# Kernel optimization log

Hardware: AMD Instinct MI355X
Metric: run time of the kernel (lower is better)

## Reference

```python
import jax, jax.numpy as jnp
import numpy as np

NUM_HEADS = 16
NUM_FEATURES = 1024
HEAD_DIM = NUM_FEATURES // NUM_HEADS
B, S = 2, 2048


def setup_inputs() -> dict:
    key = jax.random.key(0)
    ks = jax.random.split(key, 12)
    d = NUM_FEATURES
    scale = 1.0 / np.sqrt(d)
    inp = {
        'q': jax.random.normal(ks[0], (B, S, d), jnp.float32),
        'v': jax.random.normal(ks[1], (B, S, d), jnp.float32),
        'k': jax.random.normal(ks[2], (B, S, d), jnp.float32),
        'mask': jnp.ones((1, 1, S, S), jnp.float32),
        # Dense params: flax kernel layout (in, out)
        'Wq': jax.random.normal(ks[3], (d, d), jnp.float32) * scale,
        'bq': jnp.zeros((d,), jnp.float32),
        'Wv': jax.random.normal(ks[4], (d, d), jnp.float32) * scale,
        'bv': jnp.zeros((d,), jnp.float32),
        'Wk': jax.random.normal(ks[5], (d, d), jnp.float32) * scale,
        'bk': jnp.zeros((d,), jnp.float32),
        'Wo': jax.random.normal(ks[6], (d, d), jnp.float32) * scale,
        'bo': jnp.zeros((d,), jnp.float32),
    }
    return inp


def _split_heads(x):
    b, s, _ = x.shape
    return jnp.transpose(x.reshape(b, s, NUM_HEADS, HEAD_DIM), (0, 2, 1, 3))  # [B,H,S,Dh]


def reference(q, v, k, mask, Wq, bq, Wv, bv, Wk, bk, Wo, bo):
    q = q @ Wq + bq
    v = v @ Wv + bv
    k = k @ Wk + bk
    qh = _split_heads(q) / jnp.sqrt(jnp.float32(NUM_FEATURES))  # note: sqrt(d_model), as in source
    kh = _split_heads(k)
    vh = _split_heads(v)
    logits = jnp.einsum('bhqd,bhkd->bhqk', qh, kh)
    logits = logits - 1e9 * (1.0 - mask)
    weights = jax.nn.softmax(logits, axis=-1)
    # dropout deterministic (eval_mode=True) -> identity
    out = jnp.einsum('bhqk,bhkd->bhqd', weights, vh)
    out = jnp.transpose(out, (0, 2, 1, 3)).reshape(q.shape[0], q.shape[1], NUM_FEATURES)
    return out @ Wo + bo
```

## Files before the change

### kernel.cpp

```cpp
#include <hip/hip_runtime.h>
#include <hip/hip_bf16.h>


namespace {
constexpr int DM = 1024;
constexpr int NH = 16;
constexpr int HD = 64;
constexpr int SQ = 2048;
constexpr int M_TOT = 2 * SQ;

using f32x4  = __attribute__((ext_vector_type(4))) float;
using f32x16 = __attribute__((ext_vector_type(16))) float;
using bf16x8 = __attribute__((ext_vector_type(8))) short;
using u16 = unsigned short;

__device__ __forceinline__ u16 f2bf(float f) {
  union { float f; unsigned u; } x; x.f = f;
  unsigned r = x.u + 0x7fffu + ((x.u >> 16) & 1u);
  return (u16)(r >> 16);
}

__device__ __forceinline__ unsigned pk2(float lo, float hi) {
  unsigned r;
  asm("v_cvt_pk_bf16_f32 %0, %1, %2" : "=v"(r) : "v"(lo), "v"(hi));
  return r;
}

__device__ __forceinline__ float fexp2(float x) {
  float r;
  asm("v_exp_f32 %0, %1" : "=v"(r) : "v"(x));
  return r;
}

__device__ __forceinline__ f32x16 mfma32(bf16x8 a, bf16x8 b, f32x16 c) {
  return __builtin_amdgcn_mfma_f32_32x32x16_bf16(a, b, c, 0, 0, 0);
}

__device__ __forceinline__ void gld16(const void* g, void* l) {
  __builtin_amdgcn_global_load_lds((const __attribute__((address_space(1))) void*)g,
                                   (__attribute__((address_space(3))) void*)l, 16, 0, 0);
}
}

__global__ __launch_bounds__(256) void tobf_kernel(const float* __restrict__ q,
                                                   const float* __restrict__ k,
                                                   const float* __restrict__ v,
                                                   u16* __restrict__ out) {
  const float* src = blockIdx.y == 0 ? q : (blockIdx.y == 1 ? k : v);
  u16* dst = out + (size_t)blockIdx.y * M_TOT * DM;
  size_t i = ((size_t)blockIdx.x * 256 + threadIdx.x) * 8;
  float4 a = *(const float4*)(src + i), b = *(const float4*)(src + i + 4);
  union { u16 us[8]; uint4 v4; } pk;
  pk.us[0] = f2bf(a.x); pk.us[1] = f2bf(a.y); pk.us[2] = f2bf(a.z); pk.us[3] = f2bf(a.w);
  pk.us[4] = f2bf(b.x); pk.us[5] = f2bf(b.y); pk.us[6] = f2bf(b.z); pk.us[7] = f2bf(b.w);
  *(uint4*)(dst + i) = pk.v4;
}

__global__ __launch_bounds__(256) void wtrans4_kernel(const float* __restrict__ Wq,
                                                      const float* __restrict__ Wk,
                                                      const float* __restrict__ Wv,
                                                      const float* __restrict__ Wo,
                                                      u16* __restrict__ W3t,
                                                      u16* __restrict__ Wot) {
  const int z = blockIdx.z;
  const float* W = z == 0 ? Wq : (z == 1 ? Wk : (z == 2 ? Wv : Wo));
  u16* Wt = z < 3 ? W3t + (size_t)z * DM * DM : Wot;
  __shared__ u16 tile[64][65];
  const int t = threadIdx.x;
  const int k0 = blockIdx.y * 64, n0 = blockIdx.x * 64;
#pragma unroll
  for (int i = 0; i < 16; ++i) {
    int flat = t + i * 256;
    int kk = flat >> 6, nn = flat & 63;
    tile[kk][nn] = f2bf(W[(size_t)(k0 + kk) * DM + n0 + nn]);
  }
  __syncthreads();
#pragma unroll
  for (int i = 0; i < 16; ++i) {
    int flat = t + i * 256;
    int nn = flat >> 6, kk = flat & 63;
    Wt[(size_t)(n0 + nn) * DM + k0 + kk] = tile[kk][nn];
  }
}

__global__ __launch_bounds__(256) void vtrans_kernel(const u16* __restrict__ Vh,
                                                     u16* __restrict__ Vt) {
  __shared__ u16 tile[64][80];
  const int s0 = blockIdx.x * 64, bh = blockIdx.y;
  const u16* src = Vh + ((size_t)bh * SQ + s0) * HD;
  u16* dst = Vt + (size_t)bh * HD * SQ + s0;
  const int t = threadIdx.x;
#pragma unroll
  for (int i = 0; i < 2; ++i) {
    int flat = t + i * 256;
    int sr = flat >> 3, ch = flat & 7;
    *(uint4*)&tile[sr][ch * 8] = *(const uint4*)&src[(size_t)sr * HD + ch * 8];
  }
  __syncthreads();
#pragma unroll
  for (int i = 0; i < 2; ++i) {
    int flat = t + i * 256;
    int dh = flat >> 3, ch = flat & 7;
    union { u16 us[8]; uint2 h[2]; } pk;
#pragma unroll
    for (int j = 0; j < 8; ++j) pk.us[j] = tile[ch * 8 + j][dh];
#pragma unroll
    for (int kq = 0; kq < 2; ++kq) {
      int g = ch * 2 + kq;
      int gl = (g & ~3) | ((g & 1) << 1) | ((g & 2) >> 1);
      *(uint2*)&dst[(size_t)dh * SQ + gl * 4] = pk.h[kq];
    }
  }
}

template <int EPI>
__device__ __forceinline__ void gemm_core(const u16* __restrict__ A,
                                          const u16* __restrict__ Wt,
                                          const float* __restrict__ bias,
                                          void* __restrict__ C, float scale,
                                          int m0, int n0, u16* ldsA, u16* ldsB) {
  const int t = threadIdx.x;
  const int lane = t & 63, w = t >> 6;
  const int wm = w >> 1, wn = w & 1;
  const int c = lane & 15, g = lane >> 4;
  const int lr = lane >> 3, lc = lane & 7;
  f32x4 acc[2][4] = {};

  for (int k0 = 0; k0 < DM; k0 += 64) {
    __syncthreads();
#pragma unroll
    for (int j = 0; j < 2; ++j) {
      int row = w * 16 + j * 8 + lr;
      int gc = lc ^ (row & 7);
      gld16(&A[(size_t)(m0 + row) * DM + k0 + gc * 8], (char*)ldsA + w * 2048 + j * 1024);
    }
#pragma unroll
    for (int j = 0; j < 4; ++j) {
      int row = w * 32 + j * 8 + lr;
      int gc = lc ^ (row & 7);
      gld16(&Wt[(size_t)(n0 + row) * DM + k0 + gc * 8], (char*)ldsB + w * 4096 + j * 1024);
    }
    __syncthreads();
#pragma unroll
    for (int ks = 0; ks < 2; ++ks) {
      bf16x8 af[2], bfr[4];
#pragma unroll
      for (int mi = 0; mi < 2; ++mi) {
        int R = wm * 32 + mi * 16 + c;
        af[mi] = *(const bf16x8*)((const char*)ldsA + R * 128 + ((4 * ks + g) ^ (R & 7)) * 16);
      }
#pragma unroll
      for (int ni = 0; ni < 4; ++ni) {
        int R = wn * 64 + ni * 16 + c;
        bfr[ni] = *(const bf16x8*)((const char*)ldsB + R * 128 + ((4 * ks + g) ^ (R & 7)) * 16);
      }
#pragma unroll
      for (int mi = 0; mi < 2; ++mi)
#pragma unroll
        for (int ni = 0; ni < 4; ++ni)
          acc[mi][ni] =
              __builtin_amdgcn_mfma_f32_16x16x32_bf16(af[mi], bfr[ni], acc[mi][ni], 0, 0, 0);
    }
  }
  float bv_[4];
#pragma unroll
  for (int ni = 0; ni < 4; ++ni) bv_[ni] = bias[n0 + wn * 64 + ni * 16 + c];
#pragma unroll
  for (int mi = 0; mi < 2; ++mi)
#pragma unroll
    for (int ni = 0; ni < 4; ++ni)
#pragma unroll
      for (int r = 0; r < 4; ++r) {
        int m = m0 + wm * 32 + mi * 16 + g * 4 + r;
        int n = n0 + wn * 64 + ni * 16 + c;
        float val = acc[mi][ni][r] + bv_[ni];
        if (EPI == 2) {
          ((float*)C)[(size_t)m * DM + n] = val;
        } else {
          int b = m >> 11, s = m & (SQ - 1);
          int h = n >> 6, dh = n & (HD - 1);
          ((u16*)C)[((size_t)(b * NH + h) * SQ + s) * HD + dh] = f2bf(val * scale);
        }
      }
}

__global__ __launch_bounds__(256) void qkvgemm_kernel(const u16* __restrict__ QKVbf,
                                                      const u16* __restrict__ W3t,
                                                      const float* __restrict__ bq,
                                                      const float* __restrict__ bk,
                                                      const float* __restrict__ bv,
                                                      u16* __restrict__ Qh,
                                                      u16* __restrict__ Kh,
                                                      u16* __restrict__ Vh) {
  __shared__ __align__(16) u16 ldsA[64 * 64];
  __shared__ __align__(16) u16 ldsB[128 * 64];
  int bid = blockIdx.x;
  int swz = (bid & 7) * 192 + (bid >> 3);
  int which = swz >> 9;
  int sub = swz & 511;
  int mt = sub >> 3, nt = sub & 7;
  const u16* A = QKVbf + (size_t)which * M_TOT * DM;
  const u16* Wt = W3t + (size_t)which * DM * DM;
  const float* bias = which == 0 ? bq : (which == 1 ? bk : bv);
  u16* C = which == 0 ? Qh : (which == 1 ? Kh : Vh);
  float scale = which == 0 ? 0.045084222f : 1.0f;
  gemm_core<0>(A, Wt, bias, C, scale, mt * 64, nt * 128, ldsA, ldsB);
}

__global__ __launch_bounds__(256) void ogemm_kernel(const u16* __restrict__ Ob,
                                                    const u16* __restrict__ Wot,
                                                    const float* __restrict__ bo,
                                                    float* __restrict__ out) {
  __shared__ __align__(16) u16 ldsA[64 * 64];
  __shared__ __align__(16) u16 ldsB[128 * 64];
  int bid = blockIdx.x;
  int swz = (bid & 7) * 64 + (bid >> 3);
  int mt = swz >> 3, nt = swz & 7;
  gemm_core<2>(Ob, Wot, bo, out, 1.0f, mt * 64, nt * 128, ldsA, ldsB);
}

__global__ __launch_bounds__(512, 4) void fattn_kernel(const u16* __restrict__ Qh,
                                                       const u16* __restrict__ Kh,
                                                       const u16* __restrict__ Vt,
                                                       u16* __restrict__ Ob) {
  __shared__ __align__(16) u16 ldsKV[2][2][2][64 * 64];
  __shared__ float ldsML[2][8][32];
  const int t = threadIdx.x;
  const int lane = t & 63, w = t >> 6;
  const int l31 = lane & 31, hi = lane >> 5;
  const int wq = w >> 1, wk = w & 1;

  const int bid = blockIdx.x;
  const int swz = (bid & 7) * 64 + (bid >> 3);
  const int bh = swz >> 4, qb = swz & 15;
  const int q0 = qb * 128 + wq * 32;
  const u16* Qb = Qh + (size_t)bh * SQ * HD;
  const u16* Kb = Kh + (size_t)bh * SQ * HD;
  const u16* Vb = Vt + (size_t)bh * HD * SQ;
  const int keybase = wk * (SQ / 2);

  bf16x8 qf[4];
#pragma unroll
  for (int ks = 0; ks < 4; ++ks)
    qf[ks] = *(const bf16x8*)&Qb[(size_t)(q0 + l31) * HD + ks * 16 + hi * 8];

  f32x16 o0 = {}, o1 = {};
  float m_run = -3e38f, l_run = 0.f;

  auto stage = [&](int kt, int buf) {
#pragma unroll
    for (int j = 0; j < 2; ++j) {
      int r = j * 32 + wq * 8 + (lane >> 3);
      int cg = (lane & 7) ^ (r & 7);
      gld16(&Kb[(size_t)(keybase + kt * 64 + r) * HD + cg * 8],
            (char*)&ldsKV[wk][buf][0][0] + j * 4096 + wq * 1024);
      gld16(&Vb[(size_t)r * SQ + keybase + kt * 64 + cg * 8],
            (char*)&ldsKV[wk][buf][1][0] + j * 4096 + wq * 1024);
    }
  };

  stage(0, 0);
  __syncthreads();

  for (int kt = 0; kt < 16; ++kt) {
    const int cur = kt & 1;
    if (kt + 1 < 16) stage(kt + 1, cur ^ 1);

    f32x16 s0 = {}, s1 = {};
    const char* kbp = (const char*)&ldsKV[wk][cur][0][0];
#pragma unroll
    for (int ks = 0; ks < 4; ++ks) {
      int ch = ((ks * 2 + hi) ^ (l31 & 7)) * 16;
      bf16x8 k0 = *(const bf16x8*)(kbp + l31 * 128 + ch);
      bf16x8 k1 = *(const bf16x8*)(kbp + (32 + l31) * 128 + ch);
      s0 = mfma32(k0, qf[ks], s0);
      s1 = mfma32(k1, qf[ks], s1);
    }

    float mx[16];
#pragma unroll
    for (int r = 0; r < 16; ++r) mx[r] = fmaxf(s0[r], s1[r]);
#pragma unroll
    for (int d = 8; d >= 1; d >>= 1)
#pragma unroll
      for (int r = 0; r < d; ++r) mx[r] = fmaxf(mx[r], mx[r + d]);
    float pmax = fmaxf(mx[0], __shfl_xor(mx[0], 32));

    if (__any(pmax > m_run + 8.0f)) {
      float mnew = fmaxf(m_run, pmax);
      float scf = fexp2(m_run - mnew);
      m_run = mnew;
      l_run *= scf;
#pragma unroll
      for (int r = 0; r < 16; ++r) {
        float sv = __shfl(scf, (r & 3) + 8 * (r >> 2) + 4 * hi);
        o0[r] *= sv;
        o1[r] *= sv;
      }
    }
#pragma unroll
    for (int r = 0; r < 16; ++r) {
      s0[r] = fexp2(s0[r] - m_run);
      s1[r] = fexp2(s1[r] - m_run);
    }
    float sm[16];
#pragma unroll
    for (int r = 0; r < 16; ++r) sm[r] = s0[r] + s1[r];
#pragma unroll
    for (int d = 8; d >= 1; d >>= 1)
#pragma unroll
      for (int r = 0; r < d; ++r) sm[r] += sm[r + d];
    l_run += sm[0];

    union W8 { unsigned u[4]; bf16x8 v; };
    W8 pa[4];
#pragma unroll
    for (int wd = 0; wd < 4; ++wd) {
      pa[0].u[wd] = pk2(s0[2 * wd], s0[2 * wd + 1]);
      pa[1].u[wd] = pk2(s0[8 + 2 * wd], s0[9 + 2 * wd]);
      pa[2].u[wd] = pk2(s1[2 * wd], s1[2 * wd + 1]);
      pa[3].u[wd] = pk2(s1[8 + 2 * wd], s1[9 + 2 * wd]);
    }

    const char* vbp = (const char*)&ldsKV[wk][cur][1][0];
#pragma unroll
    for (int g = 0; g < 4; ++g) {
      int ch = ((g * 2 + hi) ^ (l31 & 7)) * 16;
      bf16x8 v0 = *(const bf16x8*)(vbp + l31 * 128 + ch);
      bf16x8 v1 = *(const bf16x8*)(vbp + (32 + l31) * 128 + ch);
      o0 = mfma32(pa[g].v, v0, o0);
      o1 = mfma32(pa[g].v, v1, o1);
    }

    __syncthreads();
  }

  float l2 = l_run + __shfl_xor(l_run, 32);
  float (*ldsO)[32][64] = (float(*)[32][64]) & ldsKV[0][0][0][0];
#pragma unroll
  for (int r = 0; r < 16; ++r) {
    int q = (r & 3) + 8 * (r >> 2) + 4 * hi;
    ldsO[w][q][l31] = o0[r];
    ldsO[w][q][32 + l31] = o1[r];
  }
  if (hi == 0) {
    ldsML[0][w][l31] = m_run;
    ldsML[1][w][l31] = l2;
  }
  __syncthreads();

  {
    const int q = t >> 2;
    const int dh0 = (t & 3) * 16;
    const int wA = (q >> 5) * 2;
    const int ql = q & 31;
    float m0 = ldsML[0][wA][ql], m1 = ldsML[0][wA + 1][ql];
    float l0 = ldsML[1][wA][ql], l1 = ldsML[1][wA + 1][ql];
    float mxv = fmaxf(m0, m1);
    float f0 = fexp2(m0 - mxv), f1 = fexp2(m1 - mxv);
    float inv = 1.0f / (l0 * f0 + l1 * f1);
    union { u16 us[16]; uint4 v4[2]; } pk;
#pragma unroll
    for (int j = 0; j < 16; ++j)
      pk.us[j] = f2bf((ldsO[wA][ql][dh0 + j] * f0 + ldsO[wA + 1][ql][dh0 + j] * f1) * inv);
    const int b = bh >> 4, h = bh & (NH - 1);
    size_t base = ((size_t)b * SQ + qb * 128 + q) * DM + h * HD + dh0;
    *(uint4*)&Ob[base] = pk.v4[0];
    *(uint4*)&Ob[base + 8] = pk.v4[1];
  }
}

extern "C" void kernel_launch(void* const* d_in, const int* in_sizes, int n_in,
                              void* d_out, int out_size, void* d_ws, size_t ws_size,
                              hipStream_t stream) {
  (void)in_sizes; (void)n_in; (void)out_size; (void)ws_size;
  const float* q  = (const float*)d_in[0];
  const float* v  = (const float*)d_in[1];
  const float* k  = (const float*)d_in[2];
  const float* Wq = (const float*)d_in[4];
  const float* bq = (const float*)d_in[5];
  const float* Wv = (const float*)d_in[6];
  const float* bv = (const float*)d_in[7];
  const float* Wk = (const float*)d_in[8];
  const float* bk = (const float*)d_in[9];
  const float* Wo = (const float*)d_in[10];
  const float* bo = (const float*)d_in[11];

  char* ws = (char*)d_ws;
  const size_t MB = 1024 * 1024;
  u16* W3t   = (u16*)(ws + 0 * MB);
  u16* Wot   = (u16*)(ws + 6 * MB);
  u16* QKVbf = (u16*)(ws + 8 * MB);
  u16* Vh    = (u16*)(ws + 32 * MB);
  u16* Vt    = (u16*)(ws + 8 * MB);
  u16* Ob    = (u16*)(ws + 16 * MB);
  u16* Qh    = (u16*)d_out;
  u16* Kh    = (u16*)d_out + (size_t)4 * 1024 * 1024;

  const dim3 blk(256);
  tobf_kernel<<<dim3(2048, 3), blk, 0, stream>>>(q, k, v, QKVbf);

  wtrans4_kernel<<<dim3(16, 16, 4), blk, 0, stream>>>(Wq, Wk, Wv, Wo, W3t, Wot);

  qkvgemm_kernel<<<dim3(1536), blk, 0, stream>>>(QKVbf, W3t, bq, bk, bv, Qh, Kh, Vh);

  vtrans_kernel<<<dim3(32, 32), blk, 0, stream>>>(Vh, Vt);

  fattn_kernel<<<dim3(512), dim3(512), 0, stream>>>(Qh, Kh, Vt, Ob);

  ogemm_kernel<<<dim3(512), blk, 0, stream>>>(Ob, Wot, bo, (float*)d_out);
}
```

Measured before the change: 125.8 us.

## Fuse V transpose into QKV GEMM epilogue and compute softmax row sums via MFMA

The V projection GEMM now writes its output directly in the transposed, permuted Vt layout, which removes the separate vtrans kernel launch and one round trip of V through memory. In the attention kernel, the row max reduction uses v_max3 instructions. The row-sum accumulation is moved onto the matrix cores by multiplying P with a ones vector, replacing the VALU add-reduction. The transposed epilogue stores are strided 8-byte writes, and the extra MFMAs add matrix-core work to each tile iteration.

```diff
diff --git a/kernel.cpp b/kernel.cpp
--- a/kernel.cpp
+++ b/kernel.cpp
@@ -29,6 +29,12 @@
 __device__ __forceinline__ float fexp2(float x) {
   float r;
   asm("v_exp_f32 %0, %1" : "=v"(r) : "v"(x));
+  return r;
+}
+
+__device__ __forceinline__ float m3(float a, float b, float c) {
+  float r;
+  asm("v_max3_f32 %0, %1, %2, %3" : "=v"(r) : "v"(a), "v"(b), "v"(c));
   return r;
 }
 
@@ -83,36 +89,6 @@
   }
 }
 
-__global__ __launch_bounds__(256) void vtrans_kernel(const u16* __restrict__ Vh,
-                                                     u16* __restrict__ Vt) {
-  __shared__ u16 tile[64][80];
-  const int s0 = blockIdx.x * 64, bh = blockIdx.y;
-  const u16* src = Vh + ((size_t)bh * SQ + s0) * HD;
-  u16* dst = Vt + (size_t)bh * HD * SQ + s0;
-  const int t = threadIdx.x;
-#pragma unroll
-  for (int i = 0; i < 2; ++i) {
-    int flat = t + i * 256;
-    int sr = flat >> 3, ch = flat & 7;
-    *(uint4*)&tile[sr][ch * 8] = *(const uint4*)&src[(size_t)sr * HD + ch * 8];
-  }
-  __syncthreads();
-#pragma unroll
-  for (int i = 0; i < 2; ++i) {
-    int flat = t + i * 256;
-    int dh = flat >> 3, ch = flat & 7;
-    union { u16 us[8]; uint2 h[2]; } pk;
-#pragma unroll
-    for (int j = 0; j < 8; ++j) pk.us[j] = tile[ch * 8 + j][dh];
-#pragma unroll
-    for (int kq = 0; kq < 2; ++kq) {
-      int g = ch * 2 + kq;
-      int gl = (g & ~3) | ((g & 1) << 1) | ((g & 2) >> 1);
-      *(uint2*)&dst[(size_t)dh * SQ + gl * 4] = pk.h[kq];
-    }
-  }
-}
-
 template <int EPI>
 __device__ __forceinline__ void gemm_core(const u16* __restrict__ A,
                                           const u16* __restrict__ Wt,
@@ -166,22 +142,36 @@
 #pragma unroll
   for (int ni = 0; ni < 4; ++ni) bv_[ni] = bias[n0 + wn * 64 + ni * 16 + c];
 #pragma unroll
-  for (int mi = 0; mi < 2; ++mi)
-#pragma unroll
-    for (int ni = 0; ni < 4; ++ni)
-#pragma unroll
-      for (int r = 0; r < 4; ++r) {
-        int m = m0 + wm * 32 + mi * 16 + g * 4 + r;
+  for (int mi = 0; mi < 2; ++mi) {
+#pragma unroll
+    for (int ni = 0; ni < 4; ++ni) {
+      if (EPI == 1) {
+        int mbase = m0 + wm * 32 + mi * 16 + g * 4;
         int n = n0 + wn * 64 + ni * 16 + c;
-        float val = acc[mi][ni][r] + bv_[ni];
-        if (EPI == 2) {
-          ((float*)C)[(size_t)m * DM + n] = val;
-        } else {
-          int b = m >> 11, s = m & (SQ - 1);
-          int h = n >> 6, dh = n & (HD - 1);
-          ((u16*)C)[((size_t)(b * NH + h) * SQ + s) * HD + dh] = f2bf(val * scale);
+        int b = mbase >> 11, s = mbase & (SQ - 1);
+        int sp = (s & ~12) | ((s & 4) << 1) | ((s & 8) >> 1);
+        int h = n >> 6, dh = n & (HD - 1);
+        uint2 pkd;
+        pkd.x = pk2(acc[mi][ni][0] + bv_[ni], acc[mi][ni][1] + bv_[ni]);
+        pkd.y = pk2(acc[mi][ni][2] + bv_[ni], acc[mi][ni][3] + bv_[ni]);
+        *(uint2*)&((u16*)C)[((size_t)(b * NH + h) * HD + dh) * SQ + sp] = pkd;
+      } else {
+#pragma unroll
+        for (int r = 0; r < 4; ++r) {
+          int m = m0 + wm * 32 + mi * 16 + g * 4 + r;
+          int n = n0 + wn * 64 + ni * 16 + c;
+          float val = acc[mi][ni][r] + bv_[ni];
+          if (EPI == 2) {
+            ((float*)C)[(size_t)m * DM + n] = val;
+          } else {
+            int b = m >> 11, s = m & (SQ - 1);
+            int h = n >> 6, dh = n & (HD - 1);
+            ((u16*)C)[((size_t)(b * NH + h) * SQ + s) * HD + dh] = f2bf(val * scale);
+          }
         }
       }
+    }
+  }
 }
 
 __global__ __launch_bounds__(256) void qkvgemm_kernel(const u16* __restrict__ QKVbf,
@@ -191,7 +181,7 @@
                                                       const float* __restrict__ bv,
                                                       u16* __restrict__ Qh,
                                                       u16* __restrict__ Kh,
-                                                      u16* __restrict__ Vh) {
+                                                      u16* __restrict__ Vt) {
   __shared__ __align__(16) u16 ldsA[64 * 64];
   __shared__ __align__(16) u16 ldsB[128 * 64];
   int bid = blockIdx.x;
@@ -201,10 +191,13 @@
   int mt = sub >> 3, nt = sub & 7;
   const u16* A = QKVbf + (size_t)which * M_TOT * DM;
   const u16* Wt = W3t + (size_t)which * DM * DM;
-  const float* bias = which == 0 ? bq : (which == 1 ? bk : bv);
-  u16* C = which == 0 ? Qh : (which == 1 ? Kh : Vh);
-  float scale = which == 0 ? 0.045084222f : 1.0f;
-  gemm_core<0>(A, Wt, bias, C, scale, mt * 64, nt * 128, ldsA, ldsB);
+  if (which == 0) {
+    gemm_core<0>(A, Wt, bq, Qh, 0.045084222f, mt * 64, nt * 128, ldsA, ldsB);
+  } else if (which == 1) {
+    gemm_core<0>(A, Wt, bk, Kh, 1.0f, mt * 64, nt * 128, ldsA, ldsB);
+  } else {
+    gemm_core<1>(A, Wt, bv, Vt, 1.0f, mt * 64, nt * 128, ldsA, ldsB);
+  }
 }
 
 __global__ __launch_bounds__(256) void ogemm_kernel(const u16* __restrict__ Ob,
@@ -244,8 +237,12 @@
   for (int ks = 0; ks < 4; ++ks)
     qf[ks] = *(const bf16x8*)&Qb[(size_t)(q0 + l31) * HD + ks * 16 + hi * 8];
 
+  const short ob = (short)0x3F80;
+  const bf16x8 onesv = {ob, ob, ob, ob, ob, ob, ob, ob};
+
   f32x16 o0 = {}, o1 = {};
-  float m_run = -3e38f, l_run = 0.f;
+  f32x16 lacc = {};
+  float m_run = -3e38f;
 
   auto stage = [&](int kt, int buf) {
 #pragma unroll
@@ -277,25 +274,27 @@
       s1 = mfma32(k1, qf[ks], s1);
     }
 
-    float mx[16];
-#pragma unroll
-    for (int r = 0; r < 16; ++r) mx[r] = fmaxf(s0[r], s1[r]);
-#pragma unroll
-    for (int d = 8; d >= 1; d >>= 1)
-#pragma unroll
-      for (int r = 0; r < d; ++r) mx[r] = fmaxf(mx[r], mx[r + d]);
-    float pmax = fmaxf(mx[0], __shfl_xor(mx[0], 32));
+    float t0 = m3(s0[0], s0[1], s0[2]),    t1 = m3(s0[3], s0[4], s0[5]);
+    float t2 = m3(s0[6], s0[7], s0[8]),    t3 = m3(s0[9], s0[10], s0[11]);
+    float t4 = m3(s0[12], s0[13], s0[14]), t5 = m3(s0[15], s1[0], s1[1]);
+    float t6 = m3(s1[2], s1[3], s1[4]),    t7 = m3(s1[5], s1[6], s1[7]);
+    float t8 = m3(s1[8], s1[9], s1[10]),   t9 = m3(s1[11], s1[12], s1[13]);
+    float t10 = fmaxf(s1[14], s1[15]);
+    float u0 = m3(t0, t1, t2), u1 = m3(t3, t4, t5), u2 = m3(t6, t7, t8);
+    float u3 = fmaxf(t9, t10);
+    float lm = fmaxf(m3(u0, u1, u2), u3);
+    float pmax = fmaxf(lm, __shfl_xor(lm, 32));
 
     if (__any(pmax > m_run + 8.0f)) {
       float mnew = fmaxf(m_run, pmax);
       float scf = fexp2(m_run - mnew);
       m_run = mnew;
-      l_run *= scf;
 #pragma unroll
       for (int r = 0; r < 16; ++r) {
         float sv = __shfl(scf, (r & 3) + 8 * (r >> 2) + 4 * hi);
         o0[r] *= sv;
         o1[r] *= sv;
+        lacc[r] *= sv;
       }
     }
 #pragma unroll
@@ -303,14 +302,6 @@
       s0[r] = fexp2(s0[r] - m_run);
       s1[r] = fexp2(s1[r] - m_run);
     }
-    float sm[16];
-#pragma unroll
-    for (int r = 0; r < 16; ++r) sm[r] = s0[r] + s1[r];
-#pragma unroll
-    for (int d = 8; d >= 1; d >>= 1)
-#pragma unroll
-      for (int r = 0; r < d; ++r) sm[r] += sm[r + d];
-    l_run += sm[0];
 
     union W8 { unsigned u[4]; bf16x8 v; };
     W8 pa[4];
@@ -321,6 +312,11 @@
       pa[2].u[wd] = pk2(s1[2 * wd], s1[2 * wd + 1]);
       pa[3].u[wd] = pk2(s1[8 + 2 * wd], s1[9 + 2 * wd]);
     }
+
+    lacc = mfma32(pa[0].v, onesv, lacc);
+    lacc = mfma32(pa[1].v, onesv, lacc);
+    lacc = mfma32(pa[2].v, onesv, lacc);
+    lacc = mfma32(pa[3].v, onesv, lacc);
 
     const char* vbp = (const char*)&ldsKV[wk][cur][1][0];
 #pragma unroll
@@ -335,7 +331,6 @@
     __syncthreads();
   }
 
-  float l2 = l_run + __shfl_xor(l_run, 32);
   float (*ldsO)[32][64] = (float(*)[32][64]) & ldsKV[0][0][0][0];
 #pragma unroll
   for (int r = 0; r < 16; ++r) {
@@ -343,9 +338,11 @@
     ldsO[w][q][l31] = o0[r];
     ldsO[w][q][32 + l31] = o1[r];
   }
-  if (hi == 0) {
-    ldsML[0][w][l31] = m_run;
-    ldsML[1][w][l31] = l2;
+  if (hi == 0) ldsML[0][w][l31] = m_run;
+  if (l31 == 0) {
+#pragma unroll
+    for (int r = 0; r < 16; ++r)
+      ldsML[1][w][(r & 3) + 8 * (r >> 2) + 4 * hi] = lacc[r];
   }
   __syncthreads();
 
@@ -391,8 +388,7 @@
   u16* W3t   = (u16*)(ws + 0 * MB);
   u16* Wot   = (u16*)(ws + 6 * MB);
   u16* QKVbf = (u16*)(ws + 8 * MB);
-  u16* Vh    = (u16*)(ws + 32 * MB);
-  u16* Vt    = (u16*)(ws + 8 * MB);
+  u16* Vt    = (u16*)(ws + 32 * MB);
   u16* Ob    = (u16*)(ws + 16 * MB);
   u16* Qh    = (u16*)d_out;
   u16* Kh    = (u16*)d_out + (size_t)4 * 1024 * 1024;
@@ -402,9 +398,7 @@
 
   wtrans4_kernel<<<dim3(16, 16, 4), blk, 0, stream>>>(Wq, Wk, Wv, Wo, W3t, Wot);
 
-  qkvgemm_kernel<<<dim3(1536), blk, 0, stream>>>(QKVbf, W3t, bq, bk, bv, Qh, Kh, Vh);
-
-  vtrans_kernel<<<dim3(32, 32), blk, 0, stream>>>(Vh, Vt);
+  qkvgemm_kernel<<<dim3(1536), blk, 0, stream>>>(QKVbf, W3t, bq, bk, bv, Qh, Kh, Vt);
 
   fattn_kernel<<<dim3(512), dim3(512), 0, stream>>>(Qh, Kh, Vt, Ob);
 
```

Measured after the change: 129.2 us. +2.7%, slower.
